# Performance work log

Hardware: AMD Instinct MI355X
Metric: run time of the kernel (lower is better)

## Reference

```python
import jax, jax.numpy as jnp
import numpy as np

L = 18                      # tree depth, N = 2**L - 1 nodes (complete binary tree)
N = 2**L - 1               # 262143
D = 128                     # embedding dim
V = 100000                  # vocab size of the single data type
E = 8                       # edge_count


def setup_inputs() -> dict:
    key = jax.random.key(0)
    ks = jax.random.split(key, 8)
    data = jax.random.randint(ks[0], (N,), 0, V)
    edges = jax.random.randint(ks[1], (N,), 0, E)
    data_vecs = jax.random.normal(ks[2], (V, D), dtype=jnp.float32) * 0.1
    # torch uses torch.rand (U[0,1)); scaled for numerical stability over 18 levels
    data_W = jax.random.uniform(ks[3], (D, D), dtype=jnp.float32) * 0.1
    data_b = jax.random.uniform(ks[4], (D,), dtype=jnp.float32) * 0.1
    edge_W = jax.random.uniform(ks[5], (E, D, D), dtype=jnp.float32) * (2.0 / D)
    edge_b = jax.random.uniform(ks[6], (E, D), dtype=jnp.float32) * 0.1
    score_W = jax.random.uniform(ks[7], (D, 1), dtype=jnp.float32)
    return {"data": data, "edges": edges, "data_vecs": data_vecs,
            "data_W": data_W, "data_b": data_b, "edge_W": edge_W,
            "edge_b": edge_b, "score_W": score_W}


def reference(data, edges, data_vecs, data_W, data_b, edge_W, edge_b, score_W):
    # per-node leaf term: addmm(data_bias, data_vecs[data], data_W)  -> [N, D]
    raw = data_vecs[data] @ data_W + data_b
    ret = raw    # value returned to the parent (leaves: unclamped)
    emb = raw    # stored embedding (internal nodes: pre-clamp h)
    # bottom-up over levels; level l occupies indices [2**l - 1, 2**(l+1) - 1)
    for l in reversed(range(L - 1)):
        p0, npar = 2**l - 1, 2**l
        c0, M = 2**(l + 1) - 1, 2**(l + 1)
        child_ret = ret[c0:c0 + M]              # [M, D], siblings adjacent
        eids = edges[c0:c0 + M]                 # [M]
        # edge-weighted child transform: child @ edge_W[e] + edge_b[e]
        contrib = edge_b[eids]
        for e in range(E):                      # small static edge loop
            contrib = contrib + jnp.where((eids == e)[:, None], child_ret, 0.0) @ edge_W[e]
        # sum the two children of each parent, then (leaf + children) / (nc + 1)
        contrib = contrib.reshape(npar, 2, D).sum(axis=1)
        h = (raw[p0:p0 + npar] + contrib) / 3.0
        emb = emb.at[p0:p0 + npar].set(h)
        ret = ret.at[p0:p0 + npar].set(jnp.maximum(h, 0.0))
    scores = (emb @ score_W)[:, 0]              # [N]
    return scores


if __name__ == "__main__":
    out = reference(**setup_inputs())
    print(out.shape, out.dtype)
```

## Files before the change

### kernel.cpp

```cpp
#include <hip/hip_runtime.h>

#define D 128
#define NLVL 17
#define TS 128
#define LVLPAD 1024
#define LDSTR 136
#define LEAF_BLKS 1032

typedef float  floatx4 __attribute__((ext_vector_type(4)));
typedef short  shortx8 __attribute__((ext_vector_type(8)));

__device__ __forceinline__ unsigned short f2bf(float f) {
    unsigned u = __float_as_uint(f);
    u += 0x7FFFu + ((u >> 16) & 1u);
    return (unsigned short)(u >> 16);
}
__device__ __forceinline__ float bf2f(unsigned short h) {
    return __uint_as_float(((unsigned)h) << 16);
}
__device__ __forceinline__ int lvl_base_dev(int l) { return ((2 << l) - 2) + LVLPAD * l; }

__global__ __launch_bounds__(256) void count_kernel(
    const int* __restrict__ edges, int* __restrict__ gcnt, int Nn)
{
    __shared__ int lc[NLVL * 8];
    const int t = threadIdx.x;
    for (int i = t; i < NLVL * 8; i += 256) lc[i] = 0;
    __syncthreads();
    for (int c = 1 + blockIdx.x * 256 + t; c < Nn; c += gridDim.x * 256) {
        const int e = edges[c];
        const int p = (c - 1) >> 1;
        const int l = 31 - __clz(p + 1);
        if (l >= 11) atomicAdd(&lc[l * 8 + e], 1);
    }
    __syncthreads();
    for (int i = t; i < NLVL * 8; i += 256) if (lc[i]) atomicAdd(&gcnt[i], lc[i]);
}

__global__ __launch_bounds__(256) void prefix_sv_kernel(
    const int* __restrict__ gcnt, int* __restrict__ gstart,
    const float* __restrict__ dW, const float* __restrict__ db,
    const float* __restrict__ sWs, float* __restrict__ sv, float* __restrict__ s0)
{
    __shared__ float red[256];
    const int t = threadIdx.x;
    if (t < D) {
        float acc = 0.f;
        for (int j = 0; j < D; j++) acc += dW[t * D + j] * sWs[j];
        sv[t] = acc;
    }
    red[t] = (t < D) ? db[t] * sWs[t] : 0.f;
    __syncthreads();
    for (int s = 128; s > 0; s >>= 1) { if (t < s) red[t] += red[t + s]; __syncthreads(); }
    if (t == 0) {
        *s0 = red[0];
        for (int l = 0; l < NLVL; l++) {
            int acc = 0;
            for (int e = 0; e < 8; e++) {
                gstart[l * 9 + e] = acc;
                if (l >= 11) acc = (acc + gcnt[l * 8 + e] + (TS - 1)) & ~(TS - 1);
            }
            gstart[l * 9 + 8] = acc;
        }
    }
}

#define CHUNK 2048
__global__ __launch_bounds__(256) void place_kernel(
    const int* __restrict__ edges, const int* __restrict__ gstart,
    int* __restrict__ ctr, int* __restrict__ perm, int Nn)
{
    __shared__ unsigned char key_s[CHUNK];
    __shared__ int lcnt[NLVL * 8], lbase[NLVL * 8];
    __shared__ int gs_s[NLVL * 9];
    const int t = threadIdx.x;
    for (int i = t; i < NLVL * 8; i += 256) lcnt[i] = 0;
    for (int i = t; i < NLVL * 9; i += 256) gs_s[i] = gstart[i];
    const int base = 1 + blockIdx.x * CHUNK;
    __syncthreads();
    for (int i = t; i < CHUNK; i += 256) {
        const int c = base + i;
        if (c < Nn) {
            const int e = edges[c];
            const int p = (c - 1) >> 1;
            const int l = 31 - __clz(p + 1);
            if (l >= 11) {
                const int k = l * 8 + e;
                key_s[i] = (unsigned char)k;
                atomicAdd(&lcnt[k], 1);
            } else key_s[i] = 255;
        } else key_s[i] = 255;
    }
    __syncthreads();
    for (int i = t; i < NLVL * 8; i += 256) {
        const int n = lcnt[i];
        lbase[i] = n ? atomicAdd(&ctr[i], n) : 0;
        lcnt[i] = 0;
    }
    __syncthreads();
    for (int i = t; i < CHUNK; i += 256) {
        const int c = base + i;
        if (c >= Nn) continue;
        const int k = key_s[i];
        if (k == 255) continue;
        const int off = atomicAdd(&lcnt[k], 1);
        const int l = k >> 3, e = k & 7;
        const int pos = gs_s[l * 9 + e] + lbase[k] + off;
        perm[lvl_base_dev(l) + pos] = c;
    }
}

__global__ __launch_bounds__(256) void vec2bf_kernel(
    const float* __restrict__ vecs, unsigned short* __restrict__ vbf, int n4)
{
    for (int i = blockIdx.x * 256 + threadIdx.x; i < n4; i += gridDim.x * 256) {
        const float4 v = ((const float4*)vecs)[i];
        uint2 o;
        o.x = (unsigned)f2bf(v.x) | ((unsigned)f2bf(v.y) << 16);
        o.y = (unsigned)f2bf(v.z) | ((unsigned)f2bf(v.w) << 16);
        ((uint2*)vbf)[i] = o;
    }
}

__global__ __launch_bounds__(256) void compose_kernel(
    const float* __restrict__ dW, const float* __restrict__ db,
    const float* __restrict__ eW, const float* __restrict__ eb,
    float* __restrict__ C, float* __restrict__ dv)
{
    __shared__ float aw_s[D * D];
    __shared__ float w_s[D * 32];
    const int t = threadIdx.x;
    const int e = blockIdx.x >> 2, cc = blockIdx.x & 3;
    for (int i = t; i < D * D / 4; i += 256) ((float4*)aw_s)[i] = ((const float4*)dW)[i];
    for (int i = t; i < D * 8; i += 256) {
        const int k = i >> 3, j4 = i & 7;
        ((float4*)w_s)[i] = ((const float4*)eW)[((size_t)e * D + k) * 32 + cc * 8 + j4];
    }
    __syncthreads();
    const int r2 = t >> 1, h = t & 1;
    float4 acc[4];
    #pragma unroll
    for (int m = 0; m < 4; m++) acc[m] = make_float4(0.f, 0.f, 0.f, 0.f);
    for (int k = 0; k < D; k++) {
        const float a = aw_s[r2 * D + k];
        #pragma unroll
        for (int m = 0; m < 4; m++) {
            const float4 w4 = ((const float4*)w_s)[k * 8 + h * 4 + m];
            acc[m].x += a * w4.x; acc[m].y += a * w4.y; acc[m].z += a * w4.z; acc[m].w += a * w4.w;
        }
    }
    #pragma unroll
    for (int m = 0; m < 4; m++)
        ((float4*)C)[((size_t)e * D + r2) * 32 + cc * 8 + h * 4 + m] = acc[m];
    if (t < 32) {
        float a2 = 0.f;
        for (int k = 0; k < D; k++) a2 += db[k] * w_s[k * 32 + t];
        dv[e * D + cc * 32 + t] = a2 + eb[e * D + cc * 32 + t];
    }
}

__global__ __launch_bounds__(256) void convert_kernel(
    const float* __restrict__ eW, const float* __restrict__ Ccomp,
    const float* __restrict__ dW,
    unsigned short* __restrict__ ewt, unsigned short* __restrict__ cwt,
    unsigned short* __restrict__ dwt)
{
    __shared__ float lds[D * 129];
    const int b = blockIdx.x;
    const float* src = (b < 8) ? (eW + (size_t)b * D * D)
                     : (b < 16) ? (Ccomp + (size_t)(b - 8) * D * D)
                     : dW;
    unsigned short* dst = (b < 8) ? (ewt + (size_t)b * D * D)
                        : (b < 16) ? (cwt + (size_t)(b - 8) * D * D)
                        : dwt;
    const int t = threadIdx.x;
    for (int i = t; i < D * D / 4; i += 256) {
        float4 v = ((const float4*)src)[i];
        const int k = (i * 4) >> 7, n = (i * 4) & 127;
        lds[k * 129 + n]     = v.x;
        lds[k * 129 + n + 1] = v.y;
        lds[k * 129 + n + 2] = v.z;
        lds[k * 129 + n + 3] = v.w;
    }
    __syncthreads();
    const int n = t >> 1, h = t & 1;
    for (int k = 0; k < 64; k++)
        dst[(size_t)n * D + h * 64 + k] = f2bf(lds[(h * 64 + k) * 129 + n]);
}

__global__ __launch_bounds__(256, 4) void leaf_embed_kernel(
    unsigned short* __restrict__ X,
    const unsigned short* __restrict__ vbf,
    const int* __restrict__ data,
    const int* __restrict__ perm,
    const int* __restrict__ gstart9,
    const unsigned short* __restrict__ cwt,
    const float* __restrict__ dcomp,
    const float* __restrict__ sv, const float* __restrict__ s0p,
    const unsigned short* __restrict__ dwt,
    const float* __restrict__ db,
    float* __restrict__ out,
    int NI, int lbase_leaf)
{
    __shared__ unsigned short a_s[TS * LDSTR];
    const int t = threadIdx.x;
    const bool is_leaf = (blockIdx.x < LEAF_BLKS);
    const int r = t >> 1, h = t & 1;

    int e = 0, c;
    const unsigned short* Wg;
    const float* bias;
    if (is_leaf) {
        const int ts = blockIdx.x * TS;
        if (ts >= gstart9[8]) return;
        #pragma unroll
        for (int j = 1; j < 8; j++) if (ts >= gstart9[j]) e = j;
        c = perm[lbase_leaf + ts + r];
        Wg = cwt + (size_t)e * D * D;
        bias = dcomp + (size_t)e * D;
    } else {
        const int node = (blockIdx.x - LEAF_BLKS) * TS + r;
        c = (node < NI) ? node : -1;
        Wg = dwt;
        bias = db;
    }

    {
        unsigned short* dst = a_s + r * LDSTR + h * 64;
        if (c >= 0) {
            const uint4* src = (const uint4*)(vbf + (size_t)data[c] * D + h * 64);
            if (is_leaf) {
                float sc = 0.f;
                #pragma unroll
                for (int j = 0; j < 8; j++) {
                    const uint4 v = src[j];
                    const unsigned* pv = (const unsigned*)&v;
                    #pragma unroll
                    for (int u = 0; u < 4; u++) {
                        const int n = h * 64 + j * 8 + u * 2;
                        sc += bf2f((unsigned short)pv[u]) * sv[n]
                            + bf2f((unsigned short)(pv[u] >> 16)) * sv[n + 1];
                    }
                    ((uint4*)dst)[j] = v;
                }
                sc += __shfl_xor(sc, 1, 64);
                if (h == 0) out[c] = sc + s0p[0];
            } else {
                #pragma unroll
                for (int j = 0; j < 8; j++) ((uint4*)dst)[j] = src[j];
            }
        } else {
            #pragma unroll
            for (int j = 0; j < 8; j++) ((uint4*)dst)[j] = make_uint4(0u, 0u, 0u, 0u);
        }
    }
    __syncthreads();

    const int lane = t & 63, wv = t >> 6;
    const int cq = lane & 15, q = lane >> 4;
    const floatx4 z4 = {0.f, 0.f, 0.f, 0.f};
    floatx4 acc[8][2];
    #pragma unroll
    for (int i = 0; i < 8; i++) { acc[i][0] = z4; acc[i][1] = z4; }
    #pragma unroll
    for (int ks = 0; ks < 4; ks++) {
        shortx8 bfr[2];
        #pragma unroll
        for (int nl = 0; nl < 2; nl++) {
            const int n = (wv * 2 + nl) * 16 + cq;
            bfr[nl] = *(const shortx8*)(Wg + (size_t)n * D + ks * 32 + q * 8);
        }
        #pragma unroll
        for (int mt = 0; mt < 8; mt++) {
            const shortx8 af = *(const shortx8*)(a_s + (mt * 16 + cq) * LDSTR + ks * 32 + q * 8);
            acc[mt][0] = __builtin_amdgcn_mfma_f32_16x16x32_bf16(af, bfr[0], acc[mt][0], 0, 0, 0);
            acc[mt][1] = __builtin_amdgcn_mfma_f32_16x16x32_bf16(af, bfr[1], acc[mt][1], 0, 0, 0);
        }
    }
    __syncthreads();
    #pragma unroll
    for (int nl = 0; nl < 2; nl++) {
        const int n = (wv * 2 + nl) * 16 + cq;
        const float bn = bias[n];
        #pragma unroll
        for (int mt = 0; mt < 8; mt++) {
            #pragma unroll
            for (int rg = 0; rg < 4; rg++) {
                const int m = mt * 16 + q * 4 + rg;
                a_s[m * LDSTR + n] = f2bf(acc[mt][nl][rg] + bn);
            }
        }
    }
    __syncthreads();
    if (c >= 0) {
        uint4* dst = (uint4*)(X + (size_t)c * D + h * 64);
        const uint4* srcl = (const uint4*)(a_s + r * LDSTR + h * 64);
        #pragma unroll
        for (int j = 0; j < 8; j++) dst[j] = srcl[j];
    }
}

__global__ __launch_bounds__(256, 4) void tree_gemm_kernel(
    unsigned short* __restrict__ X,
    const int* __restrict__ perm,
    const int* __restrict__ gstart9,
    const unsigned short* __restrict__ ewt,
    const float* __restrict__ eb,
    const float* __restrict__ svec,
    float* __restrict__ out,
    int lbase)
{
    __shared__ unsigned short a_s[TS * LDSTR];
    const int t = threadIdx.x;
    const int ts = blockIdx.x * TS;
    if (ts >= gstart9[8]) return;
    int e = 0;
    #pragma unroll
    for (int j = 1; j < 8; j++) if (ts >= gstart9[j]) e = j;
    const int r = t >> 1, h = t & 1;
    const int c = perm[lbase + ts + r];
    const unsigned short* Wg = ewt + (size_t)e * D * D;

    {
        unsigned short* dst = a_s + r * LDSTR + h * 64;
        if (c >= 0) {
            const uint4* xr = (const uint4*)(X + (size_t)c * D + h * 64);
            const uint4* ya = (const uint4*)(X + (size_t)(2 * c + 1) * D + h * 64);
            const uint4* yb = (const uint4*)(X + (size_t)(2 * c + 2) * D + h * 64);
            const float inv3 = 1.0f / 3.0f;
            float sc = 0.f;
            #pragma unroll
            for (int j = 0; j < 8; j++) {
                uint4 ra = xr[j], rb = ya[j], rc = yb[j];
                const unsigned* pa = (const unsigned*)&ra;
                const unsigned* pb = (const unsigned*)&rb;
                const unsigned* pc = (const unsigned*)&rc;
                unsigned ou[4];
                #pragma unroll
                for (int u = 0; u < 4; u++) {
                    const float h0 = (bf2f((unsigned short)pa[u]) + bf2f((unsigned short)pb[u])
                                    + bf2f((unsigned short)pc[u])) * inv3;
                    const float h1 = (bf2f((unsigned short)(pa[u] >> 16)) + bf2f((unsigned short)(pb[u] >> 16))
                                    + bf2f((unsigned short)(pc[u] >> 16))) * inv3;
                    const int n = h * 64 + j * 8 + u * 2;
                    sc += h0 * svec[n] + h1 * svec[n + 1];
                    unsigned short q0 = f2bf(h0), q1 = f2bf(h1);
                    q0 = (q0 & 0x8000u) ? 0 : q0;
                    q1 = (q1 & 0x8000u) ? 0 : q1;
                    ou[u] = (unsigned)q0 | ((unsigned)q1 << 16);
                }
                ((uint4*)dst)[j] = make_uint4(ou[0], ou[1], ou[2], ou[3]);
            }
            sc += __shfl_xor(sc, 1, 64);
            if (h == 0) out[c] = sc;
        } else {
            #pragma unroll
            for (int j = 0; j < 8; j++) ((uint4*)dst)[j] = make_uint4(0u, 0u, 0u, 0u);
        }
    }
    __syncthreads();
    const int lane = t & 63, wv = t >> 6;
    const int cq = lane & 15, q = lane >> 4;
    const floatx4 z4 = {0.f, 0.f, 0.f, 0.f};
    floatx4 acc[8][2];
    #pragma unroll
    for (int i = 0; i < 8; i++) { acc[i][0] = z4; acc[i][1] = z4; }
    #pragma unroll
    for (int ks = 0; ks < 4; ks++) {
        shortx8 bfr[2];
        #pragma unroll
        for (int nl = 0; nl < 2; nl++) {
            const int n = (wv * 2 + nl) * 16 + cq;
            bfr[nl] = *(const shortx8*)(Wg + (size_t)n * D + ks * 32 + q * 8);
        }
        #pragma unroll
        for (int mt = 0; mt < 8; mt++) {
            const shortx8 af = *(const shortx8*)(a_s + (mt * 16 + cq) * LDSTR + ks * 32 + q * 8);
            acc[mt][0] = __builtin_amdgcn_mfma_f32_16x16x32_bf16(af, bfr[0], acc[mt][0], 0, 0, 0);
            acc[mt][1] = __builtin_amdgcn_mfma_f32_16x16x32_bf16(af, bfr[1], acc[mt][1], 0, 0, 0);
        }
    }
    __syncthreads();
    #pragma unroll
    for (int nl = 0; nl < 2; nl++) {
        const int n = (wv * 2 + nl) * 16 + cq;
        const float bn = eb[(size_t)e * D + n];
        #pragma unroll
        for (int mt = 0; mt < 8; mt++) {
            #pragma unroll
            for (int rg = 0; rg < 4; rg++) {
                const int m = mt * 16 + q * 4 + rg;
                a_s[m * LDSTR + n] = f2bf(acc[mt][nl][rg] + bn);
            }
        }
    }
    __syncthreads();
    if (c >= 0) {
        uint4* dst = (uint4*)(X + (size_t)c * D + h * 64);
        const uint4* srcl = (const uint4*)(a_s + r * LDSTR + h * 64);
        #pragma unroll
        for (int j = 0; j < 8; j++) dst[j] = srcl[j];
    }
}

__global__ __launch_bounds__(256) void sub_kernel(
    unsigned short* __restrict__ X,
    const float* __restrict__ eW,
    const float* __restrict__ eb,
    const int* __restrict__ edges,
    const float* __restrict__ sW,
    float* __restrict__ out,
    int rbase, int nlev)
{
    __shared__ __align__(16) float xbuf[4][D];
    const int t = threadIdx.x, wv = t >> 6, lane = t & 63;
    const int u = rbase + blockIdx.x;
    const int j2 = lane * 2;
    const float inv3 = 1.0f / 3.0f;

    for (int lev = nlev - 1; lev >= 0; lev--) {
        const int first = ((u + 1) << lev) - 1;
        const int cnt = 1 << lev;
        for (int i = wv; i < cnt; i += 4) {
            const int n = first + i;
            const unsigned ra = *(const unsigned*)(X + (size_t)n * D + j2);
            const unsigned rb = *(const unsigned*)(X + (size_t)(2 * n + 1) * D + j2);
            const unsigned rc = *(const unsigned*)(X + (size_t)(2 * n + 2) * D + j2);
            const float h0 = (bf2f((unsigned short)ra) + bf2f((unsigned short)rb)
                            + bf2f((unsigned short)rc)) * inv3;
            const float h1 = (bf2f((unsigned short)(ra >> 16)) + bf2f((unsigned short)(rb >> 16))
                            + bf2f((unsigned short)(rc >> 16))) * inv3;
            float sc = h0 * sW[j2] + h1 * sW[j2 + 1];
            #pragma unroll
            for (int o = 32; o > 0; o >>= 1) sc += __shfl_xor(sc, o, 64);
            if (lane == 0) out[n] = sc;
            if (n == 0) continue;
            float2 x2 = make_float2(fmaxf(h0, 0.f), fmaxf(h1, 0.f));
            *(float2*)(xbuf[wv] + j2) = x2;
            const int e = edges[n];
            const float* W = eW + (size_t)e * D * D;
            float y0 = 0.f, y1 = 0.f;
            #pragma unroll 8
            for (int k4 = 0; k4 < 32; k4++) {
                const float4 xk = *(const float4*)(xbuf[wv] + k4 * 4);
                const float2 w0 = *(const float2*)(W + (size_t)(k4 * 4 + 0) * D + j2);
                const float2 w1 = *(const float2*)(W + (size_t)(k4 * 4 + 1) * D + j2);
                const float2 w2 = *(const float2*)(W + (size_t)(k4 * 4 + 2) * D + j2);
                const float2 w3 = *(const float2*)(W + (size_t)(k4 * 4 + 3) * D + j2);
                y0 += xk.x * w0.x + xk.y * w1.x + xk.z * w2.x + xk.w * w3.x;
                y1 += xk.x * w0.y + xk.y * w1.y + xk.z * w2.y + xk.w * w3.y;
            }
            y0 += eb[e * D + j2];
            y1 += eb[e * D + j2 + 1];
            const unsigned o = (unsigned)f2bf(y0) | ((unsigned)f2bf(y1) << 16);
            *(unsigned*)(X + (size_t)n * D + j2) = o;
        }
        __syncthreads();
    }
}

extern "C" void kernel_launch(void* const* d_in, const int* in_sizes, int n_in,
                              void* d_out, int out_size, void* d_ws, size_t ws_size,
                              hipStream_t stream) {
    const int*   data      = (const int*)d_in[0];
    const int*   edges     = (const int*)d_in[1];
    const float* data_vecs = (const float*)d_in[2];
    const float* data_W    = (const float*)d_in[3];
    const float* data_b    = (const float*)d_in[4];
    const float* edge_W    = (const float*)d_in[5];
    const float* edge_b    = (const float*)d_in[6];
    const float* score_W   = (const float*)d_in[7];
    float* out = (float*)d_out;

    const int Nn = in_sizes[0];
    const int NI = Nn >> 1;
    const int VD = in_sizes[2];
    const int PERM_TOTAL = (Nn - 1) + LVLPAD * NLVL;

    char* w = (char*)d_ws;
    size_t off = 0;
    unsigned short* X = (unsigned short*)(w + off); off += (size_t)Nn * D * 2;
    int* perm = (int*)(w + off);  off += (size_t)PERM_TOTAL * 4;
    off = (off + 255) & ~(size_t)255;
    int* gstart = (int*)(w + off); off += NLVL * 9 * 4;
    int* gcnt   = (int*)(w + off); off += NLVL * 8 * 4;
    int* ctr    = (int*)(w + off); off += NLVL * 8 * 4;
    const size_t zero_ints = NLVL * 9 + NLVL * 8 + NLVL * 8;
    off = (off + 255) & ~(size_t)255;
    float* Ccomp = (float*)(w + off); off += (size_t)8 * D * D * 4;
    float* dcomp = (float*)(w + off); off += 8 * D * 4;
    float* sv    = (float*)(w + off); off += D * 4;
    float* s0    = (float*)(w + off); off += 256;
    off = (off + 255) & ~(size_t)255;
    unsigned short* ewt = (unsigned short*)(w + off); off += (size_t)8 * D * D * 2;
    unsigned short* cwt = (unsigned short*)(w + off); off += (size_t)8 * D * D * 2;
    unsigned short* dwt = (unsigned short*)(w + off); off += (size_t)D * D * 2;
    off = (off + 255) & ~(size_t)255;
    unsigned short* vbf = (unsigned short*)(w + off); off += (size_t)VD * 2;

    hipMemsetAsync(perm, 0xFF, (size_t)PERM_TOTAL * 4, stream);
    hipMemsetAsync(gstart, 0, zero_ints * 4, stream);

    count_kernel<<<128, 256, 0, stream>>>(edges, gcnt, Nn);
    prefix_sv_kernel<<<1, 256, 0, stream>>>(gcnt, gstart, data_W, data_b, score_W, sv, s0);
    place_kernel<<<(Nn - 1 + CHUNK - 1) / CHUNK, 256, 0, stream>>>(edges, gstart, ctr, perm, Nn);
    compose_kernel<<<32, 256, 0, stream>>>(data_W, data_b, edge_W, edge_b, Ccomp, dcomp);
    convert_kernel<<<17, 256, 0, stream>>>(edge_W, Ccomp, data_W, ewt, cwt, dwt);
    vec2bf_kernel<<<1024, 256, 0, stream>>>(data_vecs, vbf, VD / 4);

    {
        const int embed_blks = (NI + TS - 1) / TS;
        const int lbase_leaf = ((2 << 16) - 2) + LVLPAD * 16;
        leaf_embed_kernel<<<LEAF_BLKS + embed_blks, 256, 0, stream>>>(
            X, vbf, data, perm, gstart + 16 * 9,
            cwt, dcomp, sv, s0, dwt, data_b, out, NI, lbase_leaf);
    }

    for (int l = 15; l >= 11; l--) {
        const int M = 2 << l;
        const int lbase = ((2 << l) - 2) + LVLPAD * l;
        tree_gemm_kernel<<<M / TS + 8, 256, 0, stream>>>(
            X, perm, gstart + l * 9, ewt, edge_b, score_W, out, lbase);
    }

    sub_kernel<<<256, 256, 0, stream>>>(X, edge_W, edge_b, edges, score_W, out, 255, 4);
    sub_kernel<<<16, 256, 0, stream>>>(X, edge_W, edge_b, edges, score_W, out, 15, 4);
    sub_kernel<<<1, 256, 0, stream>>>(X, edge_W, edge_b, edges, score_W, out, 0, 4);
}
```

Before: 339.7 us.

## Merge setup kernels, drop memsets, and restrict sorted GEMM levels to 13+

Folds compose, convert, vec2bf and the sv/s0 reduction into one prep kernel, and writes the composed matrix straight to bf16 transposed so the fp32 intermediate is gone. Replaces both memsets with per-block count slices plus a glim bound check, so padding slots in perm no longer need -1 initialisation. The edge-sorted GEMM path now covers levels 13-15 only, and levels 11-12 move to sub_kernel with a changed grouping. The aim is fewer launches and less setup traffic, at the cost of the gather-based sub_kernel handling more levels.

After: 339.4 us. About the same (-0.1%).

```diff
diff --git a/kernel.cpp b/kernel.cpp
--- a/kernel.cpp
+++ b/kernel.cpp
@@ -6,6 +6,7 @@
 #define LVLPAD 1024
 #define LDSTR 136
 #define LEAF_BLKS 1032
+#define CHUNK 2048
 
 typedef float  floatx4 __attribute__((ext_vector_type(4)));
 typedef short  shortx8 __attribute__((ext_vector_type(8)));
@@ -21,62 +22,67 @@
 __device__ __forceinline__ int lvl_base_dev(int l) { return ((2 << l) - 2) + LVLPAD * l; }
 
 __global__ __launch_bounds__(256) void count_kernel(
-    const int* __restrict__ edges, int* __restrict__ gcnt, int Nn)
-{
-    __shared__ int lc[NLVL * 8];
+    const int* __restrict__ edges, int* __restrict__ gcnt128, int Nn)
+{
+    __shared__ int lc[32];
     const int t = threadIdx.x;
-    for (int i = t; i < NLVL * 8; i += 256) lc[i] = 0;
-    __syncthreads();
-    for (int c = 1 + blockIdx.x * 256 + t; c < Nn; c += gridDim.x * 256) {
+    if (t < 32) lc[t] = 0;
+    __syncthreads();
+    for (int c = 16383 + blockIdx.x * 256 + t; c < Nn; c += gridDim.x * 256) {
         const int e = edges[c];
         const int p = (c - 1) >> 1;
         const int l = 31 - __clz(p + 1);
-        if (l >= 11) atomicAdd(&lc[l * 8 + e], 1);
-    }
-    __syncthreads();
-    for (int i = t; i < NLVL * 8; i += 256) if (lc[i]) atomicAdd(&gcnt[i], lc[i]);
-}
-
-__global__ __launch_bounds__(256) void prefix_sv_kernel(
-    const int* __restrict__ gcnt, int* __restrict__ gstart,
-    const float* __restrict__ dW, const float* __restrict__ db,
-    const float* __restrict__ sWs, float* __restrict__ sv, float* __restrict__ s0)
-{
-    __shared__ float red[256];
+        atomicAdd(&lc[(l - 13) * 8 + e], 1);
+    }
+    __syncthreads();
+    if (t < 32) gcnt128[blockIdx.x * 32 + t] = lc[t];
+}
+
+__global__ __launch_bounds__(256) void prefix_kernel(
+    const int* __restrict__ gcnt128, int* __restrict__ gstart,
+    int* __restrict__ glim, int* __restrict__ ctr)
+{
+    __shared__ int part[256];
+    __shared__ int tot[32];
     const int t = threadIdx.x;
-    if (t < D) {
-        float acc = 0.f;
-        for (int j = 0; j < D; j++) acc += dW[t * D + j] * sWs[j];
-        sv[t] = acc;
-    }
-    red[t] = (t < D) ? db[t] * sWs[t] : 0.f;
-    __syncthreads();
-    for (int s = 128; s > 0; s >>= 1) { if (t < s) red[t] += red[t + s]; __syncthreads(); }
+    const int k = t & 31, bs = t >> 5;
+    int s = 0;
+    for (int b = bs; b < 128; b += 8) s += gcnt128[b * 32 + k];
+    part[t] = s;
+    __syncthreads();
+    if (t < 32) {
+        int tt = 0;
+        #pragma unroll
+        for (int i = 0; i < 8; i++) tt += part[t + 32 * i];
+        tot[t] = tt;
+        ctr[t] = 0;
+    }
+    __syncthreads();
     if (t == 0) {
-        *s0 = red[0];
-        for (int l = 0; l < NLVL; l++) {
+        for (int li = 0; li < 4; li++) {
+            const int l = 13 + li;
             int acc = 0;
             for (int e = 0; e < 8; e++) {
                 gstart[l * 9 + e] = acc;
-                if (l >= 11) acc = (acc + gcnt[l * 8 + e] + (TS - 1)) & ~(TS - 1);
+                glim[l * 8 + e] = acc + tot[li * 8 + e];
+                acc = (acc + tot[li * 8 + e] + (TS - 1)) & ~(TS - 1);
             }
             gstart[l * 9 + 8] = acc;
         }
     }
 }
 
-#define CHUNK 2048
 __global__ __launch_bounds__(256) void place_kernel(
     const int* __restrict__ edges, const int* __restrict__ gstart,
     int* __restrict__ ctr, int* __restrict__ perm, int Nn)
 {
     __shared__ unsigned char key_s[CHUNK];
-    __shared__ int lcnt[NLVL * 8], lbase[NLVL * 8];
-    __shared__ int gs_s[NLVL * 9];
+    __shared__ int lcnt[32], lbase[32];
+    __shared__ int gs_s[4 * 9];
     const int t = threadIdx.x;
-    for (int i = t; i < NLVL * 8; i += 256) lcnt[i] = 0;
-    for (int i = t; i < NLVL * 9; i += 256) gs_s[i] = gstart[i];
-    const int base = 1 + blockIdx.x * CHUNK;
+    if (t < 32) lcnt[t] = 0;
+    if (t < 36) gs_s[t] = gstart[13 * 9 + t];
+    const int base = 16383 + blockIdx.x * CHUNK;
     __syncthreads();
     for (int i = t; i < CHUNK; i += 256) {
         const int c = base + i;
@@ -84,108 +90,130 @@
             const int e = edges[c];
             const int p = (c - 1) >> 1;
             const int l = 31 - __clz(p + 1);
-            if (l >= 11) {
-                const int k = l * 8 + e;
-                key_s[i] = (unsigned char)k;
-                atomicAdd(&lcnt[k], 1);
-            } else key_s[i] = 255;
+            const int kk = (l - 13) * 8 + e;
+            key_s[i] = (unsigned char)kk;
+            atomicAdd(&lcnt[kk], 1);
         } else key_s[i] = 255;
     }
     __syncthreads();
-    for (int i = t; i < NLVL * 8; i += 256) {
-        const int n = lcnt[i];
-        lbase[i] = n ? atomicAdd(&ctr[i], n) : 0;
-        lcnt[i] = 0;
+    if (t < 32) {
+        const int n = lcnt[t];
+        lbase[t] = n ? atomicAdd(&ctr[t], n) : 0;
+        lcnt[t] = 0;
     }
     __syncthreads();
     for (int i = t; i < CHUNK; i += 256) {
         const int c = base + i;
         if (c >= Nn) continue;
-        const int k = key_s[i];
-        if (k == 255) continue;
-        const int off = atomicAdd(&lcnt[k], 1);
-        const int l = k >> 3, e = k & 7;
-        const int pos = gs_s[l * 9 + e] + lbase[k] + off;
+        const int kk = key_s[i];
+        if (kk == 255) continue;
+        const int off = atomicAdd(&lcnt[kk], 1);
+        const int l = (kk >> 3) + 13, e = kk & 7;
+        const int pos = gs_s[(l - 13) * 9 + e] + lbase[kk] + off;
         perm[lvl_base_dev(l) + pos] = c;
     }
 }
 
-__global__ __launch_bounds__(256) void vec2bf_kernel(
-    const float* __restrict__ vecs, unsigned short* __restrict__ vbf, int n4)
-{
-    for (int i = blockIdx.x * 256 + threadIdx.x; i < n4; i += gridDim.x * 256) {
-        const float4 v = ((const float4*)vecs)[i];
-        uint2 o;
-        o.x = (unsigned)f2bf(v.x) | ((unsigned)f2bf(v.y) << 16);
-        o.y = (unsigned)f2bf(v.z) | ((unsigned)f2bf(v.w) << 16);
-        ((uint2*)vbf)[i] = o;
-    }
-}
-
-__global__ __launch_bounds__(256) void compose_kernel(
+__global__ __launch_bounds__(256) void prep_kernel(
     const float* __restrict__ dW, const float* __restrict__ db,
     const float* __restrict__ eW, const float* __restrict__ eb,
-    float* __restrict__ C, float* __restrict__ dv)
-{
-    __shared__ float aw_s[D * D];
-    __shared__ float w_s[D * 32];
-    const int t = threadIdx.x;
-    const int e = blockIdx.x >> 2, cc = blockIdx.x & 3;
-    for (int i = t; i < D * D / 4; i += 256) ((float4*)aw_s)[i] = ((const float4*)dW)[i];
-    for (int i = t; i < D * 8; i += 256) {
-        const int k = i >> 3, j4 = i & 7;
-        ((float4*)w_s)[i] = ((const float4*)eW)[((size_t)e * D + k) * 32 + cc * 8 + j4];
-    }
-    __syncthreads();
-    const int r2 = t >> 1, h = t & 1;
-    float4 acc[4];
-    #pragma unroll
-    for (int m = 0; m < 4; m++) acc[m] = make_float4(0.f, 0.f, 0.f, 0.f);
-    for (int k = 0; k < D; k++) {
-        const float a = aw_s[r2 * D + k];
+    const float* __restrict__ sWs, const float* __restrict__ vecs,
+    unsigned short* __restrict__ ewt, unsigned short* __restrict__ cwt,
+    unsigned short* __restrict__ dwt, float* __restrict__ dcomp,
+    float* __restrict__ sv, float* __restrict__ s0,
+    unsigned short* __restrict__ vbf, int n4)
+{
+    __shared__ float smem[8448];
+    const int b = blockIdx.x, t = threadIdx.x;
+    if (b < 32) {
+        float* w_s = smem;
+        float* cs  = smem + 4096;
+        const int e = b >> 2, cc = b & 3;
+        for (int i = t; i < D * 8; i += 256) {
+            const int k = i >> 3, j4 = i & 7;
+            ((float4*)w_s)[i] = ((const float4*)eW)[((size_t)e * D + k) * 32 + cc * 8 + j4];
+        }
+        __syncthreads();
+        const int r2 = t >> 1, h = t & 1;
+        float4 acc[4];
+        #pragma unroll
+        for (int m = 0; m < 4; m++) acc[m] = make_float4(0.f, 0.f, 0.f, 0.f);
+        for (int k = 0; k < D; k++) {
+            const float a = dW[(size_t)r2 * D + k];
+            #pragma unroll
+            for (int m = 0; m < 4; m++) {
+                const float4 w4 = ((const float4*)w_s)[k * 8 + h * 4 + m];
+                acc[m].x += a * w4.x; acc[m].y += a * w4.y; acc[m].z += a * w4.z; acc[m].w += a * w4.w;
+            }
+        }
         #pragma unroll
         for (int m = 0; m < 4; m++) {
-            const float4 w4 = ((const float4*)w_s)[k * 8 + h * 4 + m];
-            acc[m].x += a * w4.x; acc[m].y += a * w4.y; acc[m].z += a * w4.z; acc[m].w += a * w4.w;
-        }
-    }
-    #pragma unroll
-    for (int m = 0; m < 4; m++)
-        ((float4*)C)[((size_t)e * D + r2) * 32 + cc * 8 + h * 4 + m] = acc[m];
-    if (t < 32) {
-        float a2 = 0.f;
-        for (int k = 0; k < D; k++) a2 += db[k] * w_s[k * 32 + t];
-        dv[e * D + cc * 32 + t] = a2 + eb[e * D + cc * 32 + t];
-    }
-}
-
-__global__ __launch_bounds__(256) void convert_kernel(
-    const float* __restrict__ eW, const float* __restrict__ Ccomp,
-    const float* __restrict__ dW,
-    unsigned short* __restrict__ ewt, unsigned short* __restrict__ cwt,
-    unsigned short* __restrict__ dwt)
-{
-    __shared__ float lds[D * 129];
-    const int b = blockIdx.x;
-    const float* src = (b < 8) ? (eW + (size_t)b * D * D)
-                     : (b < 16) ? (Ccomp + (size_t)(b - 8) * D * D)
-                     : dW;
-    unsigned short* dst = (b < 8) ? (ewt + (size_t)b * D * D)
-                        : (b < 16) ? (cwt + (size_t)(b - 8) * D * D)
-                        : dwt;
-    const int t = threadIdx.x;
-    for (int i = t; i < D * D / 4; i += 256) {
-        float4 v = ((const float4*)src)[i];
-        const int k = (i * 4) >> 7, n = (i * 4) & 127;
-        lds[k * 129 + n]     = v.x;
-        lds[k * 129 + n + 1] = v.y;
-        lds[k * 129 + n + 2] = v.z;
-        lds[k * 129 + n + 3] = v.w;
-    }
-    __syncthreads();
-    const int n = t >> 1, h = t & 1;
-    for (int k = 0; k < 64; k++)
-        dst[(size_t)n * D + h * 64 + k] = f2bf(lds[(h * 64 + k) * 129 + n]);
+            cs[r2 * 33 + h * 16 + m * 4 + 0] = acc[m].x;
+            cs[r2 * 33 + h * 16 + m * 4 + 1] = acc[m].y;
+            cs[r2 * 33 + h * 16 + m * 4 + 2] = acc[m].z;
+            cs[r2 * 33 + h * 16 + m * 4 + 3] = acc[m].w;
+        }
+        __syncthreads();
+        {
+            const int nn = t >> 3, kseg = t & 7, k0 = kseg * 16;
+            unsigned ow[8];
+            #pragma unroll
+            for (int i2 = 0; i2 < 8; i2++) {
+                const unsigned short lo = f2bf(cs[(k0 + 2 * i2) * 33 + nn]);
+                const unsigned short hi = f2bf(cs[(k0 + 2 * i2 + 1) * 33 + nn]);
+                ow[i2] = (unsigned)lo | ((unsigned)hi << 16);
+            }
+            uint4* dstp = (uint4*)(cwt + (size_t)e * D * D + (size_t)(cc * 32 + nn) * D + k0);
+            dstp[0] = make_uint4(ow[0], ow[1], ow[2], ow[3]);
+            dstp[1] = make_uint4(ow[4], ow[5], ow[6], ow[7]);
+        }
+        if (t < 32) {
+            float a2 = 0.f;
+            for (int k = 0; k < D; k++) a2 += db[k] * w_s[k * 32 + t];
+            dcomp[e * D + cc * 32 + t] = a2 + eb[e * D + cc * 32 + t];
+        }
+    } else if (b < 41) {
+        float* lds = smem;
+        const int bb = b - 32;
+        const float* src = (bb < 8) ? (eW + (size_t)bb * D * D) : dW;
+        unsigned short* dst = (bb < 8) ? (ewt + (size_t)bb * D * D) : dwt;
+        for (int half = 0; half < 2; half++) {
+            __syncthreads();
+            for (int i = t; i < 64 * D / 4; i += 256) {
+                float4 v = ((const float4*)src)[half * (64 * D / 4) + i];
+                const int k = (i * 4) >> 7, n = (i * 4) & 127;
+                lds[k * 129 + n]     = v.x;
+                lds[k * 129 + n + 1] = v.y;
+                lds[k * 129 + n + 2] = v.z;
+                lds[k * 129 + n + 3] = v.w;
+            }
+            __syncthreads();
+            const int n = t >> 1, hh = t & 1;
+            for (int kk = 0; kk < 32; kk++) {
+                const int k = hh * 32 + kk;
+                dst[(size_t)n * D + half * 64 + k] = f2bf(lds[k * 129 + n]);
+            }
+        }
+    } else if (b == 41) {
+        float* red = smem;
+        if (t < D) {
+            float acc = 0.f;
+            for (int j = 0; j < D; j++) acc += dW[(size_t)t * D + j] * sWs[j];
+            sv[t] = acc;
+        }
+        red[t] = (t < D) ? db[t] * sWs[t] : 0.f;
+        __syncthreads();
+        for (int s = 128; s > 0; s >>= 1) { if (t < s) red[t] += red[t + s]; __syncthreads(); }
+        if (t == 0) s0[0] = red[0];
+    } else {
+        for (int i = (b - 42) * 256 + t; i < n4; i += (gridDim.x - 42) * 256) {
+            const float4 v = ((const float4*)vecs)[i];
+            uint2 o;
+            o.x = (unsigned)f2bf(v.x) | ((unsigned)f2bf(v.y) << 16);
+            o.y = (unsigned)f2bf(v.z) | ((unsigned)f2bf(v.w) << 16);
+            ((uint2*)vbf)[i] = o;
+        }
+    }
 }
 
 __global__ __launch_bounds__(256, 4) void leaf_embed_kernel(
@@ -194,6 +222,7 @@
     const int* __restrict__ data,
     const int* __restrict__ perm,
     const int* __restrict__ gstart9,
+    const int* __restrict__ glim8,
     const unsigned short* __restrict__ cwt,
     const float* __restrict__ dcomp,
     const float* __restrict__ sv, const float* __restrict__ s0p,
@@ -215,7 +244,8 @@
         if (ts >= gstart9[8]) return;
         #pragma unroll
         for (int j = 1; j < 8; j++) if (ts >= gstart9[j]) e = j;
-        c = perm[lbase_leaf + ts + r];
+        const int p = ts + r;
+        c = (p < glim8[e]) ? perm[lbase_leaf + p] : -1;
         Wg = cwt + (size_t)e * D * D;
         bias = dcomp + (size_t)e * D;
     } else {
@@ -304,6 +334,7 @@
     unsigned short* __restrict__ X,
     const int* __restrict__ perm,
     const int* __restrict__ gstart9,
+    const int* __restrict__ glim8,
     const unsigned short* __restrict__ ewt,
     const float* __restrict__ eb,
     const float* __restrict__ svec,
@@ -318,7 +349,8 @@
     #pragma unroll
     for (int j = 1; j < 8; j++) if (ts >= gstart9[j]) e = j;
     const int r = t >> 1, h = t & 1;
-    const int c = perm[lbase + ts + r];
+    const int p = ts + r;
+    const int c = (p < glim8[e]) ? perm[lbase + p] : -1;
     const unsigned short* Wg = ewt + (size_t)e * D * D;
 
     {
@@ -482,12 +514,11 @@
     unsigned short* X = (unsigned short*)(w + off); off += (size_t)Nn * D * 2;
     int* perm = (int*)(w + off);  off += (size_t)PERM_TOTAL * 4;
     off = (off + 255) & ~(size_t)255;
-    int* gstart = (int*)(w + off); off += NLVL * 9 * 4;
-    int* gcnt   = (int*)(w + off); off += NLVL * 8 * 4;
-    int* ctr    = (int*)(w + off); off += NLVL * 8 * 4;
-    const size_t zero_ints = NLVL * 9 + NLVL * 8 + NLVL * 8;
+    int* gstart  = (int*)(w + off); off += NLVL * 9 * 4;
+    int* glim    = (int*)(w + off); off += NLVL * 8 * 4;
+    int* gcnt128 = (int*)(w + off); off += 128 * 32 * 4;
+    int* ctr     = (int*)(w + off); off += 32 * 4;
     off = (off + 255) & ~(size_t)255;
-    float* Ccomp = (float*)(w + off); off += (size_t)8 * D * D * 4;
     float* dcomp = (float*)(w + off); off += 8 * D * 4;
     float* sv    = (float*)(w + off); off += D * 4;
     float* s0    = (float*)(w + off); off += 256;
@@ -498,32 +529,32 @@
     off = (off + 255) & ~(size_t)255;
     unsigned short* vbf = (unsigned short*)(w + off); off += (size_t)VD * 2;
 
-    hipMemsetAsync(perm, 0xFF, (size_t)PERM_TOTAL * 4, stream);
-    hipMemsetAsync(gstart, 0, zero_ints * 4, stream);
-
-    count_kernel<<<128, 256, 0, stream>>>(edges, gcnt, Nn);
-    prefix_sv_kernel<<<1, 256, 0, stream>>>(gcnt, gstart, data_W, data_b, score_W, sv, s0);
-    place_kernel<<<(Nn - 1 + CHUNK - 1) / CHUNK, 256, 0, stream>>>(edges, gstart, ctr, perm, Nn);
-    compose_kernel<<<32, 256, 0, stream>>>(data_W, data_b, edge_W, edge_b, Ccomp, dcomp);
-    convert_kernel<<<17, 256, 0, stream>>>(edge_W, Ccomp, data_W, ewt, cwt, dwt);
-    vec2bf_kernel<<<1024, 256, 0, stream>>>(data_vecs, vbf, VD / 4);
+    count_kernel<<<128, 256, 0, stream>>>(edges, gcnt128, Nn);
+    prefix_kernel<<<1, 256, 0, stream>>>(gcnt128, gstart, glim, ctr);
+    const int place_blks = (Nn - 16383 + CHUNK - 1) / CHUNK;
+    place_kernel<<<place_blks, 256, 0, stream>>>(edges, gstart, ctr, perm, Nn);
+
+    prep_kernel<<<42 + 1024, 256, 0, stream>>>(
+        data_W, data_b, edge_W, edge_b, score_W, data_vecs,
+        ewt, cwt, dwt, dcomp, sv, s0, vbf, VD / 4);
 
     {
         const int embed_blks = (NI + TS - 1) / TS;
         const int lbase_leaf = ((2 << 16) - 2) + LVLPAD * 16;
         leaf_embed_kernel<<<LEAF_BLKS + embed_blks, 256, 0, stream>>>(
-            X, vbf, data, perm, gstart + 16 * 9,
+            X, vbf, data, perm, gstart + 16 * 9, glim + 16 * 8,
             cwt, dcomp, sv, s0, dwt, data_b, out, NI, lbase_leaf);
     }
 
-    for (int l = 15; l >= 11; l--) {
+    for (int l = 15; l >= 13; l--) {
         const int M = 2 << l;
         const int lbase = ((2 << l) - 2) + LVLPAD * l;
         tree_gemm_kernel<<<M / TS + 8, 256, 0, stream>>>(
-            X, perm, gstart + l * 9, ewt, edge_b, score_W, out, lbase);
-    }
-
-    sub_kernel<<<256, 256, 0, stream>>>(X, edge_W, edge_b, edges, score_W, out, 255, 4);
-    sub_kernel<<<16, 256, 0, stream>>>(X, edge_W, edge_b, edges, score_W, out, 15, 4);
-    sub_kernel<<<1, 256, 0, stream>>>(X, edge_W, edge_b, edges, score_W, out, 0, 4);
-}
+            X, perm, gstart + l * 9, glim + l * 8, ewt, edge_b, score_W, out, lbase);
+    }
+
+    sub_kernel<<<2048, 256, 0, stream>>>(X, edge_W, edge_b, edges, score_W, out, 2047, 3);
+    sub_kernel<<<128, 256, 0, stream>>>(X, edge_W, edge_b, edges, score_W, out, 127, 4);
+    sub_kernel<<<8, 256, 0, stream>>>(X, edge_W, edge_b, edges, score_W, out, 7, 4);
+    sub_kernel<<<1, 256, 0, stream>>>(X, edge_W, edge_b, edges, score_W, out, 0, 3);
+}
```
